# Optimization experiments

Measured on AMD Instinct MI355X. Metric: run time of the kernel, lower is better.

## Reference

```python
import jax, jax.numpy as jnp
import numpy as np

N, E, DIN, D, FE, L, B, M = 10000, 40000, 11, 64, 4, 4, 512, 3


def setup_inputs() -> dict:
    key = jax.random.key(0)
    ks = iter(jax.random.split(key, 24))
    s = lambda *sh: jax.random.normal(next(ks), sh, jnp.float32)
    return {
        "x": s(N, DIN),
        "edge_index": jax.random.randint(next(ks), (2, E), 0, N),
        "edge_attr": jax.random.uniform(next(ks), (E, FE), jnp.float32),
        "batch": jnp.sort(jax.random.randint(next(ks), (N,), 0, B)),
        "W0": s(DIN, D) * 0.1, "b0": jnp.zeros((D,), jnp.float32),
        "Wn1": s(FE, 2 * D) * 0.1, "bn1": jnp.zeros((2 * D,), jnp.float32),
        "Wn2": s(2 * D, D * D) * 0.02, "bn2": jnp.zeros((D * D,), jnp.float32),
        "root": s(L, D, D) * 0.1, "conv_bias": jnp.zeros((L, D), jnp.float32),
        "lstm_Wih": s(4 * D, 2 * D) * 0.1, "lstm_Whh": s(4 * D, D) * 0.1,
        "lstm_b": jnp.zeros((4 * D,), jnp.float32),
        "Wo1": s(2 * D, D) * 0.1, "bo1": jnp.zeros((D,), jnp.float32),
        "Wo2": s(D, 1) * 0.1, "bo2": jnp.zeros((1,), jnp.float32),
    }


def reference(x, edge_index, edge_attr, batch, W0, b0, Wn1, bn1, Wn2, bn2,
              root, conv_bias, lstm_Wih, lstm_Whh, lstm_b, Wo1, bo1, Wo2, bo2):
    src, dst = edge_index[0], edge_index[1]
    h = x @ W0 + b0  # [N, D]
    # Edge MLP is SHARED across all conv layers -> compute per-edge weight matrices once
    ew = (jax.nn.silu(edge_attr @ Wn1 + bn1) @ Wn2 + bn2).reshape(E, D, D)
    for l in range(L):
        msg = jnp.einsum('ed,edf->ef', h[src], ew)  # gather-compute per edge
        aggr = jax.ops.segment_sum(msg, dst, num_segments=N)  # scatter-add to targets
        h = h + (aggr + h @ root[l] + conv_bias[l])  # NNConv + residual
    # Set2Set pooling (LSTM, M processing steps)
    q_star = jnp.zeros((B, 2 * D), h.dtype)
    hs = jnp.zeros((B, D), h.dtype)
    cs = jnp.zeros((B, D), h.dtype)
    for _ in range(M):
        gates = q_star @ lstm_Wih.T + hs @ lstm_Whh.T + lstm_b
        i, f, g, o = jnp.split(gates, 4, axis=-1)  # torch LSTM gate order
        cs = jax.nn.sigmoid(f) * cs + jax.nn.sigmoid(i) * jnp.tanh(g)
        hs = jax.nn.sigmoid(o) * jnp.tanh(cs)
        q = hs  # [B, D]
        e = jnp.sum(h * q[batch], axis=-1)  # [N]
        emax = jax.ops.segment_max(e, batch, num_segments=B)
        ex = jnp.exp(e - emax[batch])
        denom = jax.ops.segment_sum(ex, batch, num_segments=B)
        a = ex / denom[batch]  # per-graph softmax attention
        r = jax.ops.segment_sum(a[:, None] * h, batch, num_segments=B)
        q_star = jnp.concatenate([q, r], axis=-1)
    out = jax.nn.silu(q_star @ Wo1 + bo1) @ Wo2 + bo2
    return out.reshape(-1)
```

## Files before the change

kernel.cpp:

```cpp
#include <hip/hip_runtime.h>
#include <cstdint>
#include <cstddef>

#define NN   10000
#define EE   40000
#define DIN_ 11
#define DD   64
#define LL   4
#define BB   512
#define MM   3
#define K1   128
#define DD2  4096
#define NPB  10

typedef unsigned short ushort_t;
typedef unsigned int   uint_t;

typedef __bf16 bf16x8_t __attribute__((ext_vector_type(8)));
typedef float  f32x4_t  __attribute__((ext_vector_type(4)));
union FragU { uint4 u; bf16x8_t b; };

__device__ __forceinline__ float bfu(ushort_t u) { return __uint_as_float(((uint_t)u) << 16); }
__device__ __forceinline__ float bflo(uint_t u) { return __uint_as_float(u << 16); }
__device__ __forceinline__ float bfhi(uint_t u) { return __uint_as_float(u & 0xffff0000u); }
__device__ __forceinline__ ushort_t f2bf(float f) {
  uint_t u = __float_as_uint(f);
  u = (u + 0x7fffu + ((u >> 16) & 1u)) >> 16;
  return (ushort_t)u;
}
__device__ __forceinline__ uint_t pack2(float lo, float hi) {
  return (uint_t)f2bf(lo) | ((uint_t)f2bf(hi) << 16);
}
__device__ __forceinline__ float sigmf_(float x) { return 1.f / (1.f + expf(-x)); }
__device__ __forceinline__ float siluf_(float x) { return x / (1.f + expf(-x)); }

#if defined(__HIP_DEVICE_COMPILE__) && __has_builtin(__builtin_amdgcn_fdot2_f32_bf16)
typedef __bf16 bf16x2_t __attribute__((ext_vector_type(2)));
__device__ __forceinline__ float dot2a(uint_t a, uint_t b, float c) {
  union { uint_t u; bf16x2_t v; } ua, ub;
  ua.u = a; ub.u = b;
  return __builtin_amdgcn_fdot2_f32_bf16(ua.v, ub.v, c, false);
}
#else
__device__ __forceinline__ float dot2a(uint_t a, uint_t b, float c) {
  return c + bflo(a) * bflo(b) + bfhi(a) * bfhi(b);
}
#endif

__global__ void k_detect(const ushort_t* __restrict__ ea, int* __restrict__ flag) {
  __shared__ int bad;
  if (threadIdx.x == 0) bad = 0;
  __syncthreads();
  ushort_t u = ea[threadIdx.x];
  if ((u & 0x8000u) || u > 0x3F80u) atomicAdd(&bad, 1);
  __syncthreads();
  if (threadIdx.x == 0) *flag = (bad == 0) ? 1 : 0;
}

#define NCANON 16
struct CanonArgs {
  const void* src[NCANON];
  float* dst[NCANON];
  int n[NCANON];
};
__global__ void k_canon(CanonArgs a, const int* __restrict__ flag) {
  const int ai = blockIdx.y;
  const int n = a.n[ai];
  const int i = blockIdx.x * 256 + threadIdx.x;
  if (i >= n) return;
  float v;
  if (*flag) v = bfu(((const ushort_t*)a.src[ai])[i]);
  else       v = ((const float*)a.src[ai])[i];
  a.dst[ai][i] = v;
}

__global__ void k_wn2m(const void* __restrict__ Wn2, uint_t* __restrict__ out,
                       const int* __restrict__ flag) {
  int o = blockIdx.x * 256 + threadIdx.x;
  if (o >= 64 * 4 * 2 * 2 * 64 * 4) return;
  int jp = o & 3; int r = o >> 2;
  int lane = r & 63; r >>= 6;
  int hf = r & 1; r >>= 1;
  int par = r & 1; r >>= 1;
  int fc = r & 3; r >>= 2;
  int kpg = r;
  int q = lane >> 4, n = lane & 15;
  int d0 = hf * 32 + q * 8 + 2 * jp;
  int f = fc * 16 + n;
  int k = kpg * 2 + par;
  size_t c0 = (size_t)k * DD2 + d0 * 64 + f;
  size_t c1 = c0 + 64;
  uint_t lo, hi;
  if (*flag) {
    const ushort_t* s = (const ushort_t*)Wn2;
    lo = s[c0]; hi = s[c1];
  } else {
    const float* s = (const float*)Wn2;
    lo = f2bf(s[c0]); hi = f2bf(s[c1]);
  }
  out[o] = lo | (hi << 16);
}

__global__ void k_wT(const float* __restrict__ Wihc, const float* __restrict__ Whhc,
                     float* __restrict__ Wiht, float* __restrict__ Whht) {
  int idx = blockIdx.x * 256 + threadIdx.x;
  if (idx < 4 * DD * K1) {
    int j = idx >> 7, i = idx & 127;
    Wiht[i * 256 + j] = Wihc[idx];
  }
  if (idx < 4 * DD * DD) {
    int j = idx >> 6, i = idx & 63;
    Whht[i * 256 + j] = Whhc[idx];
  }
}

__global__ void k_embed(const float* __restrict__ x, const float* __restrict__ W0,
                        const float* __restrict__ b0, const float* __restrict__ bn2,
                        float* __restrict__ h, uint_t* __restrict__ hpk,
                        float* __restrict__ nbias) {
  __shared__ float xs[DIN_];
  __shared__ float hl[DD];
  const int n = blockIdx.x, f = threadIdx.x;
  if (f < DIN_) xs[f] = x[n * DIN_ + f];
  __syncthreads();
  float a = b0[f];
  for (int i = 0; i < DIN_; ++i) a += xs[i] * W0[i * DD + f];
  h[(size_t)n * DD + f] = a;
  hl[f] = a;
  float other = __shfl_down(a, 1);
  if ((f & 1) == 0)
    hpk[(size_t)n * 32 + (f >> 1)] = pack2(a, other);
  __syncthreads();
  float nb = 0.f;
#pragma unroll
  for (int d = 0; d < DD; ++d) nb += hl[d] * bn2[d * DD + f];
  nbias[(size_t)n * DD + f] = nb;
}

__global__ void k_edgemlp(const float* __restrict__ ea, const float* __restrict__ Wn1,
                          const float* __restrict__ bn1, const int* __restrict__ epos,
                          uint_t* __restrict__ hn1s) {
  int idx = blockIdx.x * 256 + threadIdx.x;
  if (idx >= EE * (K1 / 2)) return;
  int e = idx >> 6, j = idx & 63;
  int k0 = 2 * j, k1 = 2 * j + 1;
  float a0 = ea[e * 4 + 0], a1 = ea[e * 4 + 1], a2 = ea[e * 4 + 2], a3 = ea[e * 4 + 3];
  float t0 = bn1[k0] + a0 * Wn1[k0] + a1 * Wn1[K1 + k0] + a2 * Wn1[2 * K1 + k0] + a3 * Wn1[3 * K1 + k0];
  float t1 = bn1[k1] + a0 * Wn1[k1] + a1 * Wn1[K1 + k1] + a2 * Wn1[2 * K1 + k1] + a3 * Wn1[3 * K1 + k1];
  int pos = epos[e];
  hn1s[(size_t)pos * 64 + j] = pack2(siluf_(t0), siluf_(t1));
}

__global__ void k_hist(const int* __restrict__ ei, int* __restrict__ cnt_s) {
  int e = blockIdx.x * 256 + threadIdx.x;
  if (e >= EE) return;
  atomicAdd(&cnt_s[ei[e]], 1);
}

__global__ void k_scan(const int* __restrict__ cnt, int* __restrict__ rp) {
  __shared__ int part[1024];
  const int tid = threadIdx.x;
  const int chunk = (NN + 1023) / 1024;
  int s = 0;
  for (int j = 0; j < chunk; ++j) {
    int idx = tid * chunk + j;
    if (idx < NN) s += cnt[idx];
  }
  part[tid] = s;
  __syncthreads();
  for (int off = 1; off < 1024; off <<= 1) {
    int v = (tid >= off) ? part[tid - off] : 0;
    __syncthreads();
    part[tid] += v;
    __syncthreads();
  }
  int base = (tid == 0) ? 0 : part[tid - 1];
  for (int j = 0; j < chunk; ++j) {
    int idx = tid * chunk + j;
    if (idx < NN) { rp[idx] = base; base += cnt[idx]; }
  }
  if (tid == 1023) rp[NN] = part[1023];
}

__global__ void k_fill(const int* __restrict__ ei, const int* __restrict__ rps,
                       int* __restrict__ cur_s, int* __restrict__ epos,
                       int* __restrict__ esd) {
  int e = blockIdx.x * 256 + threadIdx.x;
  if (e >= EE) return;
  int s = ei[e], d = ei[EE + e];
  int ps = atomicAdd(&cur_s[s], 1);
  int pos = rps[s] + ps;
  epos[e] = pos;
  esd[2 * pos] = s;
  esd[2 * pos + 1] = d;
}

__global__ void k_goff(const int* __restrict__ batch, int* __restrict__ goff) {
  int g = blockIdx.x * 256 + threadIdx.x;
  if (g > BB) return;
  int lo = 0, hi = NN;
  while (lo < hi) {
    int mid = (lo + hi) >> 1;
    if (batch[mid] < g) lo = mid + 1; else hi = mid;
  }
  goff[g] = lo;
}

__global__ __launch_bounds__(256, 4) void k_conv(
    const uint_t* __restrict__ hpk, const uint_t* __restrict__ hn1s,
    const uint_t* __restrict__ Wn2m, const float* __restrict__ nbias,
    const int* __restrict__ rps, const int* __restrict__ esd,
    float* __restrict__ aggr) {
  __shared__ uint_t Gp[NPB * 4 * 64 * 4];
  const int tid = threadIdx.x;
  const int w = tid >> 6, lane = tid & 63;
  const int q = lane >> 4, n16 = lane & 15;
  const int n0 = blockIdx.x * NPB;

  FragU a0, a1;
  {
    int nn = n0 + n16;
    if (nn > NN - 1) nn = NN - 1;
    const uint4* ap = (const uint4*)(hpk + (size_t)nn * 32);
    a0.u = ap[q];
    a1.u = ap[4 + q];
  }
  const int e0 = rps[n0], e1 = rps[n0 + NPB];

  for (int c = 0; c < 4; ++c) {
    if (c) __syncthreads();
    for (int fc = 0; fc < 4; ++fc) {
      uint_t pk[4][4];
#pragma unroll
      for (int kk = 0; kk < 4; ++kk) {
        const int kpg = c * 16 + w * 4 + kk;
        const uint4* bp = (const uint4*)Wn2m + (size_t)(kpg * 4 + fc) * 256 + lane;
        FragU b00, b01, b10, b11;
        b00.u = bp[0];
        b01.u = bp[64];
        b10.u = bp[128];
        b11.u = bp[192];
        f32x4_t acc0 = {0.f, 0.f, 0.f, 0.f};
        f32x4_t acc1 = {0.f, 0.f, 0.f, 0.f};
        acc0 = __builtin_amdgcn_mfma_f32_16x16x32_bf16(a0.b, b00.b, acc0, 0, 0, 0);
        acc0 = __builtin_amdgcn_mfma_f32_16x16x32_bf16(a1.b, b01.b, acc0, 0, 0, 0);
        acc1 = __builtin_amdgcn_mfma_f32_16x16x32_bf16(a0.b, b10.b, acc1, 0, 0, 0);
        acc1 = __builtin_amdgcn_mfma_f32_16x16x32_bf16(a1.b, b11.b, acc1, 0, 0, 0);
#pragma unroll
        for (int r = 0; r < 4; ++r)
          pk[kk][r] = pack2(acc0[r], acc1[r]);
      }
#pragma unroll
      for (int r = 0; r < 4; ++r) {
        const int m = q * 4 + r;
        if (m < NPB) {
          uint4 v;
          v.x = pk[0][r]; v.y = pk[1][r]; v.z = pk[2][r]; v.w = pk[3][r];
          ((uint4*)Gp)[(m * 4 + w) * 64 + fc * 16 + n16] = v;
        }
      }
    }
    __syncthreads();
    for (int ii = e0 + w; ii < e1; ii += 4) {
      const int iiu = __builtin_amdgcn_readfirstlane(ii);
      const int src = __builtin_amdgcn_readfirstlane(esd[2 * iiu]);
      const int dst = __builtin_amdgcn_readfirstlane(esd[2 * iiu + 1]);
      const int m = src - n0;
      float p = (c == 0) ? nbias[(size_t)src * 64 + lane] : 0.f;
      const uint4* hp = (const uint4*)(hn1s + (size_t)iiu * 64 + c * 16);
      const uint4* gb = (const uint4*)Gp + (size_t)m * 256 + lane;
#pragma unroll
      for (int kpq = 0; kpq < 4; ++kpq) {
        uint4 gv = gb[kpq * 64];
        uint4 hv = hp[kpq];
        p = dot2a(gv.x, hv.x, p);
        p = dot2a(gv.y, hv.y, p);
        p = dot2a(gv.z, hv.z, p);
        p = dot2a(gv.w, hv.w, p);
      }
      atomicAdd(&aggr[(size_t)dst * 64 + lane], p);
    }
  }
}

__global__ void k_update(float* __restrict__ h, uint_t* __restrict__ hpk,
                         float* __restrict__ aggr, const float* __restrict__ bn2,
                         const float* __restrict__ root, const float* __restrict__ cb,
                         float* __restrict__ nbias, int l) {
  __shared__ float hl[DD];
  const int n = blockIdx.x, f = threadIdx.x;
  hl[f] = h[(size_t)n * DD + f];
  __syncthreads();
  float acc = hl[f] + aggr[(size_t)n * DD + f] + cb[l * DD + f];
  aggr[(size_t)n * DD + f] = 0.f;
  const float* rp = root + (size_t)l * DD2 + f;
#pragma unroll
  for (int d = 0; d < DD; ++d) acc += hl[d] * rp[d * DD];
  h[(size_t)n * DD + f] = acc;
  float other = __shfl_down(acc, 1);
  if ((f & 1) == 0)
    hpk[(size_t)n * 32 + (f >> 1)] = pack2(acc, other);
  __syncthreads();
  hl[f] = acc;
  __syncthreads();
  float nb = 0.f;
#pragma unroll
  for (int d = 0; d < DD; ++d) nb += hl[d] * bn2[d * DD + f];
  nbias[(size_t)n * DD + f] = nb;
}

#define EVCAP 2048
__global__ void k_s2s(const float* __restrict__ h, const int* __restrict__ goff,
                      const float* __restrict__ Wiht, const float* __restrict__ Whht,
                      const float* __restrict__ lb,
                      const float* __restrict__ Wo1, const float* __restrict__ bo1,
                      const float* __restrict__ Wo2, const float* __restrict__ bo2,
                      void* __restrict__ outv, const int* __restrict__ flag) {
  __shared__ float qsl[K1];
  __shared__ float hsl[DD];
  __shared__ float csl[DD];
  __shared__ float gl[4][DD];
  __shared__ float red[256];
  __shared__ float ev[EVCAP];
  __shared__ float rp4[4][DD];
  const int g = blockIdx.x, tid = threadIdx.x;

  if (tid < K1) qsl[tid] = 0.f;
  else if (tid < K1 + DD) hsl[tid - K1] = 0.f;
  else csl[tid - K1 - DD] = 0.f;
  __syncthreads();

  const int i0 = goff[g];
  int cnt = goff[g + 1] - i0;
  if (cnt > EVCAP) cnt = EVCAP;

  for (int m = 0; m < MM; ++m) {
    {
      float a = lb[tid];
      for (int i = 0; i < K1; ++i) a += qsl[i] * Wiht[i * 256 + tid];
      for (int i = 0; i < DD; ++i) a += hsl[i] * Whht[i * 256 + tid];
      gl[tid >> 6][tid & 63] = a;
    }
    __syncthreads();
    if (tid < DD) {
      float ig = sigmf_(gl[0][tid]), fg = sigmf_(gl[1][tid]);
      float gg = tanhf(gl[2][tid]), og = sigmf_(gl[3][tid]);
      float c = fg * csl[tid] + ig * gg;
      csl[tid] = c;
      hsl[tid] = og * tanhf(c);
    }
    __syncthreads();
    float lmax = -1e30f;
    for (int jj = tid; jj < cnt; jj += 256) {
      const float* hp = h + (size_t)(i0 + jj) * DD;
      float e = 0.f;
#pragma unroll
      for (int d = 0; d < DD; ++d) e += hp[d] * hsl[d];
      ev[jj] = e;
      lmax = fmaxf(lmax, e);
    }
    red[tid] = lmax;
    __syncthreads();
    for (int s = 128; s > 0; s >>= 1) {
      if (tid < s) red[tid] = fmaxf(red[tid], red[tid + s]);
      __syncthreads();
    }
    const float emax = red[0];
    __syncthreads();
    float lsum = 0.f;
    for (int jj = tid; jj < cnt; jj += 256) {
      float ex = expf(ev[jj] - emax);
      ev[jj] = ex;
      lsum += ex;
    }
    red[tid] = lsum;
    __syncthreads();
    for (int s = 128; s > 0; s >>= 1) {
      if (tid < s) red[tid] += red[tid + s];
      __syncthreads();
    }
    const float denom = red[0];
    const int f = tid & 63, grp = tid >> 6;
    float acc = 0.f;
    for (int jj = grp; jj < cnt; jj += 4)
      acc += ev[jj] * h[(size_t)(i0 + jj) * DD + f];
    rp4[grp][f] = acc;
    __syncthreads();
    if (tid < DD) {
      float r = rp4[0][tid] + rp4[1][tid] + rp4[2][tid] + rp4[3][tid];
      r = (cnt > 0 && denom > 0.f) ? r / denom : 0.f;
      qsl[tid] = hsl[tid];
      qsl[DD + tid] = r;
    }
    __syncthreads();
  }
  if (tid < DD) {
    float t = bo1[tid];
    for (int i = 0; i < K1; ++i) t += qsl[i] * Wo1[i * DD + tid];
    float s = siluf_(t) * Wo2[tid];
    for (int off = 32; off > 0; off >>= 1) s += __shfl_down(s, off);
    if (tid == 0) {
      float v = s + bo2[0];
      if (*flag) ((ushort_t*)outv)[g] = f2bf(v);
      else       ((float*)outv)[g] = v;
    }
  }
}

extern "C" void kernel_launch(void* const* d_in, const int* in_sizes, int n_in,
                              void* d_out, int out_size, void* d_ws, size_t ws_size,
                              hipStream_t stream) {
  const void* x_r    = d_in[0];
  const int*  ei     = (const int*)d_in[1];
  const void* ea_r   = d_in[2];
  const int*  batch  = (const int*)d_in[3];
  const void* W0_r   = d_in[4];
  const void* b0_r   = d_in[5];
  const void* Wn1_r  = d_in[6];
  const void* bn1_r  = d_in[7];
  const void* Wn2_r  = d_in[8];
  const void* bn2_r  = d_in[9];
  const void* root_r = d_in[10];
  const void* cb_r   = d_in[11];
  const void* Wih_r  = d_in[12];
  const void* Whh_r  = d_in[13];
  const void* lb_r   = d_in[14];
  const void* Wo1_r  = d_in[15];
  const void* bo1_r  = d_in[16];
  const void* Wo2_r  = d_in[17];
  const void* bo2_r  = d_in[18];

  char* w = (char*)d_ws;
  size_t off = 0;
  auto alloc = [&](size_t bytes) -> void* {
    void* p = w + off;
    off = (off + bytes + 255) & ~(size_t)255;
    return p;
  };
  int* flag = (int*)alloc(4);
  float* xc    = (float*)alloc((size_t)NN * DIN_ * 4);
  float* eac   = (float*)alloc((size_t)EE * 4 * 4);
  float* W0c   = (float*)alloc((size_t)DIN_ * DD * 4);
  float* b0c   = (float*)alloc((size_t)DD * 4);
  float* Wn1c  = (float*)alloc((size_t)4 * K1 * 4);
  float* bn1c  = (float*)alloc((size_t)K1 * 4);
  float* bn2c  = (float*)alloc((size_t)DD2 * 4);
  float* rootc = (float*)alloc((size_t)LL * DD2 * 4);
  float* cbc   = (float*)alloc((size_t)LL * DD * 4);
  float* Wihc  = (float*)alloc((size_t)4 * DD * K1 * 4);
  float* Whhc  = (float*)alloc((size_t)4 * DD * DD * 4);
  float* lbc   = (float*)alloc((size_t)4 * DD * 4);
  float* Wo1c  = (float*)alloc((size_t)K1 * DD * 4);
  float* bo1c  = (float*)alloc((size_t)DD * 4);
  float* Wo2c  = (float*)alloc((size_t)DD * 4);
  float* bo2c  = (float*)alloc((size_t)4);
  float* Wiht  = (float*)alloc((size_t)K1 * 256 * 4);
  float* Whht  = (float*)alloc((size_t)DD * 256 * 4);
  uint_t* Wn2m = (uint_t*)alloc((size_t)64 * 4 * 2 * 2 * 64 * 4 * 4);
  float*  h    = (float*)alloc((size_t)NN * DD * 4);
  uint_t* hpk  = (uint_t*)alloc((size_t)NN * 32 * 4);
  uint_t* hn1s = (uint_t*)alloc((size_t)EE * (K1 / 2) * 4);
  float*  aggr = (float*)alloc((size_t)NN * DD * 4);
  float*  nbias= (float*)alloc((size_t)NN * DD * 4);
  int* cnts  = (int*)alloc((size_t)2 * NN * 4);
  int* rps   = (int*)alloc((size_t)(NN + 1) * 4);
  int* epos  = (int*)alloc((size_t)EE * 4);
  int* esd   = (int*)alloc((size_t)2 * EE * 4);
  int* goff  = (int*)alloc((size_t)(BB + 1) * 4);

  int* cnt_s = cnts;
  int* cur_s = cnts + NN;

  hipMemsetAsync(cnts, 0, (size_t)2 * NN * 4, stream);
  hipMemsetAsync(aggr, 0, (size_t)NN * DD * 4, stream);

  k_detect<<<1, 256, 0, stream>>>((const ushort_t*)ea_r, flag);

  CanonArgs ca;
  const void* srcs[NCANON] = {x_r, ea_r, W0_r, b0_r, Wn1_r, bn1_r, bn2_r, root_r,
                              cb_r, Wih_r, Whh_r, lb_r, Wo1_r, bo1_r, Wo2_r, bo2_r};
  float* dsts[NCANON] = {xc, eac, W0c, b0c, Wn1c, bn1c, bn2c, rootc,
                         cbc, Wihc, Whhc, lbc, Wo1c, bo1c, Wo2c, bo2c};
  int cnts_c[NCANON] = {NN * DIN_, EE * 4, DIN_ * DD, DD, 4 * K1, K1, DD2, LL * DD2,
                        LL * DD, 4 * DD * K1, 4 * DD * DD, 4 * DD, K1 * DD, DD, DD, 1};
  for (int i = 0; i < NCANON; ++i) { ca.src[i] = srcs[i]; ca.dst[i] = dsts[i]; ca.n[i] = cnts_c[i]; }
  {
    dim3 grid((EE * 4 + 255) / 256, NCANON);
    k_canon<<<grid, 256, 0, stream>>>(ca, flag);
  }
  k_wn2m<<<1024, 256, 0, stream>>>(Wn2_r, Wn2m, flag);
  k_wT<<<(4 * DD * K1 + 255) / 256, 256, 0, stream>>>(Wihc, Whhc, Wiht, Whht);

  k_embed<<<NN, DD, 0, stream>>>(xc, W0c, b0c, bn2c, h, hpk, nbias);
  k_hist<<<(EE + 255) / 256, 256, 0, stream>>>(ei, cnt_s);
  k_scan<<<1, 1024, 0, stream>>>(cnt_s, rps);
  k_fill<<<(EE + 255) / 256, 256, 0, stream>>>(ei, rps, cur_s, epos, esd);
  k_goff<<<(BB + 1 + 255) / 256, 256, 0, stream>>>(batch, goff);
  k_edgemlp<<<(EE * (K1 / 2) + 255) / 256, 256, 0, stream>>>(eac, Wn1c, bn1c, epos, hn1s);

  for (int l = 0; l < LL; ++l) {
    k_conv<<<NN / NPB, 256, 0, stream>>>(hpk, hn1s, Wn2m, nbias, rps, esd, aggr);
    k_update<<<NN, DD, 0, stream>>>(h, hpk, aggr, bn2c, rootc, cbc, nbias, l);
  }

  k_s2s<<<BB, 256, 0, stream>>>(h, goff, Wiht, Whht, lbc, Wo1c, bo1c, Wo2c, bo2c,
                                d_out, flag);
}
```

Measured before the change: 491.6 us.

## Fill all 16 MFMA rows per conv block, batch node updates, coalesce Wn2 repack

The conv kernel now handles 16 nodes per block instead of 10, so every row of the 16x16 MFMA tile does useful work. It also drops the row clamp and splits the K dimension into 8 smaller chunks, halving the shared-memory staging buffer so more blocks can be resident (launch bounds raised to 5 per SIMD). This cuts wasted matrix work and the number of blocks that reload weights, but doubles the barriers and edge-loop passes per block. k_update now processes 4 nodes per 256-thread block, and the Wn2 repack stages one weight row in shared memory so its global reads are coalesced.

```diff
diff --git a/kernel.cpp b/kernel.cpp
--- a/kernel.cpp
+++ b/kernel.cpp
@@ -11,7 +11,7 @@
 #define MM   3
 #define K1   128
 #define DD2  4096
-#define NPB  10
+#define NPB  16
 
 typedef unsigned short ushort_t;
 typedef unsigned int   uint_t;
@@ -76,29 +76,29 @@
 
 __global__ void k_wn2m(const void* __restrict__ Wn2, uint_t* __restrict__ out,
                        const int* __restrict__ flag) {
-  int o = blockIdx.x * 256 + threadIdx.x;
-  if (o >= 64 * 4 * 2 * 2 * 64 * 4) return;
-  int jp = o & 3; int r = o >> 2;
-  int lane = r & 63; r >>= 6;
-  int hf = r & 1; r >>= 1;
-  int par = r & 1; r >>= 1;
-  int fc = r & 3; r >>= 2;
-  int kpg = r;
-  int q = lane >> 4, n = lane & 15;
-  int d0 = hf * 32 + q * 8 + 2 * jp;
-  int f = fc * 16 + n;
-  int k = kpg * 2 + par;
-  size_t c0 = (size_t)k * DD2 + d0 * 64 + f;
-  size_t c1 = c0 + 64;
-  uint_t lo, hi;
+  __shared__ ushort_t row[DD2];
+  const int k = blockIdx.x, tid = threadIdx.x;
   if (*flag) {
-    const ushort_t* s = (const ushort_t*)Wn2;
-    lo = s[c0]; hi = s[c1];
+    const uint4* src = (const uint4*)((const ushort_t*)Wn2 + (size_t)k * DD2);
+    ((uint4*)row)[tid] = src[tid];
+    ((uint4*)row)[tid + 256] = src[tid + 256];
   } else {
-    const float* s = (const float*)Wn2;
-    lo = f2bf(s[c0]); hi = f2bf(s[c1]);
-  }
-  out[o] = lo | (hi << 16);
+    const float* src = (const float*)Wn2 + (size_t)k * DD2;
+    for (int j = 0; j < 16; ++j) row[tid + 256 * j] = f2bf(src[tid + 256 * j]);
+  }
+  __syncthreads();
+  const int kpg = k >> 1, par = k & 1;
+  const int lane = tid >> 2, jp = tid & 3;
+  const int q = lane >> 4, n = lane & 15;
+  for (int fc = 0; fc < 4; ++fc) {
+#pragma unroll
+    for (int hf = 0; hf < 2; ++hf) {
+      int d0 = hf * 32 + q * 8 + 2 * jp;
+      int f = fc * 16 + n;
+      uint_t lo = row[d0 * 64 + f], hi = row[(d0 + 1) * 64 + f];
+      out[((((size_t)kpg * 4 + fc) * 2 + par) * 2 + hf) * 256 + tid] = lo | (hi << 16);
+    }
+  }
 }
 
 __global__ void k_wT(const float* __restrict__ Wihc, const float* __restrict__ Whhc,
@@ -206,34 +206,33 @@
   goff[g] = lo;
 }
 
-__global__ __launch_bounds__(256, 4) void k_conv(
+__global__ __launch_bounds__(256, 5) void k_conv(
     const uint_t* __restrict__ hpk, const uint_t* __restrict__ hn1s,
     const uint_t* __restrict__ Wn2m, const float* __restrict__ nbias,
     const int* __restrict__ rps, const int* __restrict__ esd,
     float* __restrict__ aggr) {
-  __shared__ uint_t Gp[NPB * 4 * 64 * 4];
+  __shared__ uint_t Gp[NPB * 2 * 64 * 4];
   const int tid = threadIdx.x;
   const int w = tid >> 6, lane = tid & 63;
   const int q = lane >> 4, n16 = lane & 15;
   const int n0 = blockIdx.x * NPB;
+  const int half = w >> 1, slot2 = (w & 1) * 2;
 
   FragU a0, a1;
   {
-    int nn = n0 + n16;
-    if (nn > NN - 1) nn = NN - 1;
-    const uint4* ap = (const uint4*)(hpk + (size_t)nn * 32);
+    const uint4* ap = (const uint4*)(hpk + (size_t)(n0 + n16) * 32);
     a0.u = ap[q];
     a1.u = ap[4 + q];
   }
   const int e0 = rps[n0], e1 = rps[n0 + NPB];
 
-  for (int c = 0; c < 4; ++c) {
+  for (int c = 0; c < 8; ++c) {
     if (c) __syncthreads();
     for (int fc = 0; fc < 4; ++fc) {
-      uint_t pk[4][4];
-#pragma unroll
-      for (int kk = 0; kk < 4; ++kk) {
-        const int kpg = c * 16 + w * 4 + kk;
+      uint_t pk[2][4];
+#pragma unroll
+      for (int kk = 0; kk < 2; ++kk) {
+        const int kpg = c * 8 + 2 * w + kk;
         const uint4* bp = (const uint4*)Wn2m + (size_t)(kpg * 4 + fc) * 256 + lane;
         FragU b00, b01, b10, b11;
         b00.u = bp[0];
@@ -253,11 +252,8 @@
 #pragma unroll
       for (int r = 0; r < 4; ++r) {
         const int m = q * 4 + r;
-        if (m < NPB) {
-          uint4 v;
-          v.x = pk[0][r]; v.y = pk[1][r]; v.z = pk[2][r]; v.w = pk[3][r];
-          ((uint4*)Gp)[(m * 4 + w) * 64 + fc * 16 + n16] = v;
-        }
+        uint2 v; v.x = pk[0][r]; v.y = pk[1][r];
+        *(uint2*)&Gp[(((m * 2 + half) * 64 + fc * 16 + n16) * 4 + slot2)] = v;
       }
     }
     __syncthreads();
@@ -267,45 +263,49 @@
       const int dst = __builtin_amdgcn_readfirstlane(esd[2 * iiu + 1]);
       const int m = src - n0;
       float p = (c == 0) ? nbias[(size_t)src * 64 + lane] : 0.f;
-      const uint4* hp = (const uint4*)(hn1s + (size_t)iiu * 64 + c * 16);
-      const uint4* gb = (const uint4*)Gp + (size_t)m * 256 + lane;
-#pragma unroll
-      for (int kpq = 0; kpq < 4; ++kpq) {
-        uint4 gv = gb[kpq * 64];
-        uint4 hv = hp[kpq];
-        p = dot2a(gv.x, hv.x, p);
-        p = dot2a(gv.y, hv.y, p);
-        p = dot2a(gv.z, hv.z, p);
-        p = dot2a(gv.w, hv.w, p);
-      }
+      const uint4* hp = (const uint4*)(hn1s + (size_t)iiu * 64 + c * 8);
+      uint4 hv0 = hp[0], hv1 = hp[1];
+      const uint4* gb = (const uint4*)Gp + (size_t)(m * 2) * 64 + lane;
+      uint4 g0 = gb[0], g1 = gb[64];
+      p = dot2a(g0.x, hv0.x, p);
+      p = dot2a(g0.y, hv0.y, p);
+      p = dot2a(g0.z, hv0.z, p);
+      p = dot2a(g0.w, hv0.w, p);
+      p = dot2a(g1.x, hv1.x, p);
+      p = dot2a(g1.y, hv1.y, p);
+      p = dot2a(g1.z, hv1.z, p);
+      p = dot2a(g1.w, hv1.w, p);
       atomicAdd(&aggr[(size_t)dst * 64 + lane], p);
     }
   }
 }
 
-__global__ void k_update(float* __restrict__ h, uint_t* __restrict__ hpk,
-                         float* __restrict__ aggr, const float* __restrict__ bn2,
-                         const float* __restrict__ root, const float* __restrict__ cb,
-                         float* __restrict__ nbias, int l) {
-  __shared__ float hl[DD];
-  const int n = blockIdx.x, f = threadIdx.x;
-  hl[f] = h[(size_t)n * DD + f];
-  __syncthreads();
-  float acc = hl[f] + aggr[(size_t)n * DD + f] + cb[l * DD + f];
+__global__ __launch_bounds__(256) void k_update(
+    float* __restrict__ h, uint_t* __restrict__ hpk,
+    float* __restrict__ aggr, const float* __restrict__ bn2,
+    const float* __restrict__ root, const float* __restrict__ cb,
+    float* __restrict__ nbias, int l) {
+  __shared__ float hl[4][DD];
+  __shared__ float al[4][DD];
+  const int tid = threadIdx.x, w = tid >> 6, f = tid & 63;
+  const int n = blockIdx.x * 4 + w;
+  float hv = h[(size_t)n * DD + f];
+  hl[w][f] = hv;
+  float acc = hv + aggr[(size_t)n * DD + f] + cb[l * DD + f];
   aggr[(size_t)n * DD + f] = 0.f;
-  const float* rp = root + (size_t)l * DD2 + f;
-#pragma unroll
-  for (int d = 0; d < DD; ++d) acc += hl[d] * rp[d * DD];
+  __syncthreads();
+  const float* rp = root + (size_t)l * DD2;
+#pragma unroll
+  for (int d = 0; d < DD; ++d) acc += hl[w][d] * rp[d * DD + f];
   h[(size_t)n * DD + f] = acc;
+  al[w][f] = acc;
   float other = __shfl_down(acc, 1);
   if ((f & 1) == 0)
     hpk[(size_t)n * 32 + (f >> 1)] = pack2(acc, other);
   __syncthreads();
-  hl[f] = acc;
-  __syncthreads();
   float nb = 0.f;
 #pragma unroll
-  for (int d = 0; d < DD; ++d) nb += hl[d] * bn2[d * DD + f];
+  for (int d = 0; d < DD; ++d) nb += al[w][d] * bn2[d * DD + f];
   nbias[(size_t)n * DD + f] = nb;
 }
 
@@ -488,7 +488,7 @@
     dim3 grid((EE * 4 + 255) / 256, NCANON);
     k_canon<<<grid, 256, 0, stream>>>(ca, flag);
   }
-  k_wn2m<<<1024, 256, 0, stream>>>(Wn2_r, Wn2m, flag);
+  k_wn2m<<<K1, 256, 0, stream>>>(Wn2_r, Wn2m, flag);
   k_wT<<<(4 * DD * K1 + 255) / 256, 256, 0, stream>>>(Wihc, Whhc, Wiht, Whht);
 
   k_embed<<<NN, DD, 0, stream>>>(xc, W0c, b0c, bn2c, h, hpk, nbias);
@@ -500,7 +500,7 @@
 
   for (int l = 0; l < LL; ++l) {
     k_conv<<<NN / NPB, 256, 0, stream>>>(hpk, hn1s, Wn2m, nbias, rps, esd, aggr);
-    k_update<<<NN, DD, 0, stream>>>(h, hpk, aggr, bn2c, rootc, cbc, nbias, l);
+    k_update<<<NN / 4, 256, 0, stream>>>(h, hpk, aggr, bn2c, rootc, cbc, nbias, l);
   }
 
   k_s2s<<<BB, 256, 0, stream>>>(h, goff, Wiht, Whht, lbc, Wo1c, bo1c, Wo2c, bo2c,
```

Measured after the change: 651.6 us. +32.5%, slower.
